# Kernel optimization log

Hardware: AMD Instinct MI355X
Metric: run time of the kernel (lower is better)

## Reference

```python
import math
import jax, jax.numpy as jnp
import numpy as np

V_NODES = 100000
N_EDGES = 1600000
EMBED = 768
HID = 256
H = 4
FH = HID // H
L = 2
PE_D = EMBED // 4  # 192
SLOPE = 0.2


def make_pe(max_len, d):
    pos = np.arange(max_len, dtype=np.float32)[:, None]
    div = np.exp(np.arange(0, d, 2, dtype=np.float32) * (-math.log(10000.0) / d))
    pe = np.zeros((max_len, d), dtype=np.float32)
    pe[:, 0::2] = np.sin(pos * div)
    pe[:, 1::2] = np.cos(pos * div)
    return jnp.asarray(pe)


def setup_inputs() -> dict:
    key = jax.random.key(0)
    ks = jax.random.split(key, 24)

    def xavier(k, shape):
        fan_in, fan_out = shape[0], shape[1]
        lim = math.sqrt(6.0 / (fan_in + fan_out))
        return jax.random.uniform(k, shape, jnp.float32, -lim, lim)

    in_proj_dim = EMBED + 2 * PE_D  # 1152
    inp = {
        'row_idx': jax.random.randint(ks[0], (V_NODES,), 0, 256),
        'col_idx': jax.random.randint(ks[1], (V_NODES,), 0, 64),
        'edge_index': jax.random.randint(ks[2], (2, N_EDGES), 0, V_NODES),
        'edge_weight': jax.random.uniform(ks[3], (N_EDGES,), jnp.float32),
        'W_in': xavier(ks[4], (in_proj_dim, HID)),
        'b_in': jnp.zeros((HID,), jnp.float32),
        'ln_g': jnp.ones((HID,), jnp.float32),
        'ln_b': jnp.zeros((HID,), jnp.float32),
        'Wq': jnp.stack([xavier(ks[5 + i], (HID, HID)) for i in range(L)]),
        'bq': jnp.zeros((L, HID), jnp.float32),
        'Wk': jnp.stack([xavier(ks[7 + i], (HID, HID)) for i in range(L)]),
        'bk': jnp.zeros((L, HID), jnp.float32),
        'Wv': jnp.stack([xavier(ks[9 + i], (HID, HID)) for i in range(L)]),
        'bv': jnp.zeros((L, HID), jnp.float32),
        'Wo': jnp.stack([xavier(ks[11 + i], (HID, HID)) for i in range(L)]),
        'bo': jnp.zeros((L, HID), jnp.float32),
        'We': jnp.stack([xavier(ks[13 + i], (1, H)) for i in range(L)]),  # edge_proj weight [1,H]
        'be': jnp.zeros((L, H), jnp.float32),
    }
    return inp


def gat_layer(h, src, tgt, ew, Wq, bq, Wk, bk, Wv, bv, Wo, bo, We, be):
    V = h.shape[0]
    Q = (h @ Wq + bq).reshape(V, H, FH)
    K = (h @ Wk + bk).reshape(V, H, FH)
    Vo = (h @ Wv + bv).reshape(V, H, FH)
    # edge bias: Linear(1,H) on edge_weight, then leaky relu -> [E,H]
    edge_bias = jax.nn.leaky_relu(ew[:, None] * We.reshape(1, H) + be, SLOPE)
    attn_raw = jnp.sum(Q[src] * K[tgt], axis=-1) / math.sqrt(FH) + edge_bias  # [E,H]
    attn_exp = jnp.exp(attn_raw)
    deg = jax.ops.segment_sum(attn_exp, tgt, num_segments=V) + 1e-16  # [V,H]
    attn_norm = attn_exp / deg[tgt]  # [E,H] (dropout is identity at eval)
    msg = Vo[src] * attn_norm[:, :, None] * ew[:, None, None]  # [E,H,FH]
    out = jax.ops.segment_sum(msg, tgt, num_segments=V).reshape(V, H * FH)
    return jax.nn.leaky_relu(out @ Wo + bo, SLOPE)


def reference(row_idx, col_idx, edge_index, edge_weight,
              W_in, b_in, ln_g, ln_b,
              Wq, bq, Wk, bk, Wv, bv, Wo, bo, We, be):
    V = row_idx.shape[0]
    row_pe = make_pe(256, PE_D)
    col_pe = make_pe(64, PE_D)
    cell = jnp.zeros((V, EMBED), jnp.float32)  # cell_embeds are zeros in source
    h = jnp.concatenate([cell, row_pe[row_idx], col_pe[col_idx]], axis=-1)
    # input_proj: Linear -> LayerNorm -> ReLU (dropout identity)
    h = h @ W_in + b_in
    mu = jnp.mean(h, axis=-1, keepdims=True)
    var = jnp.var(h, axis=-1, keepdims=True)
    h = (h - mu) / jnp.sqrt(var + 1e-5) * ln_g + ln_b
    h = jax.nn.relu(h)
    src, tgt = edge_index[0], edge_index[1]
    for i in range(L):
        h = gat_layer(h, src, tgt, edge_weight,
                      Wq[i], bq[i], Wk[i], bk[i], Wv[i], bv[i],
                      Wo[i], bo[i], We[i], be[i])
    return h
```

## Files before the change

### kernel.cpp

```cpp
#include <hip/hip_runtime.h>
#include <hip/hip_bf16.h>
#include <type_traits>
#include <math.h>

typedef __attribute__((ext_vector_type(8))) short bf16x8;
typedef __attribute__((ext_vector_type(4))) float f32x4;

__device__ __forceinline__ float bf2f(unsigned int u16) {
    union { unsigned int i; float f; } x; x.i = (u16 & 0xffffu) << 16; return x.f;
}
__device__ __forceinline__ unsigned int f2bf(float f) {
    union { float f; unsigned int i; } x; x.f = f;
    unsigned int i = x.i;
    unsigned int r = i + 0x7fffu + ((i >> 16) & 1u);
    return r >> 16;
}

#define SLOPE 0.2f

__global__ void k_hist(const int* __restrict__ tgt, int* __restrict__ cnt, int E) {
    int i = blockIdx.x * blockDim.x + threadIdx.x;
    if (i < E) atomicAdd(&cnt[tgt[i]], 1);
}

__global__ void __launch_bounds__(1024) k_scan1(const int* __restrict__ in, int* __restrict__ out,
                                                int* __restrict__ bsums, int n) {
    __shared__ int sm[1024];
    int i = blockIdx.x * 1024 + threadIdx.x;
    int v = (i < n) ? in[i] : 0;
    sm[threadIdx.x] = v; __syncthreads();
    for (int ofs = 1; ofs < 1024; ofs <<= 1) {
        int t = (threadIdx.x >= ofs) ? sm[threadIdx.x - ofs] : 0;
        __syncthreads();
        sm[threadIdx.x] += t;
        __syncthreads();
    }
    if (i < n) out[i] = sm[threadIdx.x];
    if (threadIdx.x == 1023) bsums[blockIdx.x] = sm[1023];
}

__global__ void __launch_bounds__(1024) k_scan2(int* bsums, int nb) {
    __shared__ int sm[1024];
    int v = (threadIdx.x < nb) ? bsums[threadIdx.x] : 0;
    sm[threadIdx.x] = v; __syncthreads();
    for (int ofs = 1; ofs < 1024; ofs <<= 1) {
        int t = (threadIdx.x >= ofs) ? sm[threadIdx.x - ofs] : 0;
        __syncthreads();
        sm[threadIdx.x] += t;
        __syncthreads();
    }
    if (threadIdx.x < nb) bsums[threadIdx.x] = sm[threadIdx.x] - v;
}

__global__ void __launch_bounds__(1024) k_scan3(int* __restrict__ out1, const int* __restrict__ bsums,
                                                int* __restrict__ off0, int n) {
    int i = blockIdx.x * 1024 + threadIdx.x;
    if (i < n) out1[i] += bsums[blockIdx.x];
    if (i == 0) off0[0] = 0;
}

__global__ void k_scatter(const int* __restrict__ ei, const float* __restrict__ ew,
                          const int* __restrict__ off, int* __restrict__ fill,
                          int* __restrict__ ssrc, float* __restrict__ sew, int E) {
    int e = blockIdx.x * blockDim.x + threadIdx.x;
    if (e < E) {
        int s = ei[e], t = ei[E + e];
        int pos = off[t] + atomicAdd(&fill[t], 1);
        ssrc[pos] = s; sew[pos] = ew[e];
    }
}

__global__ void k_combo(const int* __restrict__ ri, const int* __restrict__ ci,
                        int* __restrict__ combo, int V) {
    int v = blockIdx.x * blockDim.x + threadIdx.x;
    if (v < V) combo[v] = ri[v] * 64 + ci[v];
}

__global__ void __launch_bounds__(256) k_wt(const float* __restrict__ Wq, const float* __restrict__ Wk,
                                            const float* __restrict__ Wv, const float* __restrict__ Wo,
                                            unsigned short* __restrict__ WT) {
    __shared__ float sm[64][65];
    int blk = blockIdx.x;
    int m = blk >> 4, t = blk & 15;
    int tr = t >> 2, tc = t & 3;
    const float* srcs[4] = {Wq, Wk, Wv, Wo};
    const float* W = srcs[m & 3] + (size_t)(m >> 2) * 65536;
    int tid = threadIdx.x;
    for (int i = tid; i < 4096; i += 256) {
        int r = i >> 6, c = i & 63;
        sm[r][c] = W[(size_t)(tr * 64 + r) * 256 + tc * 64 + c];
    }
    __syncthreads();
    for (int i = tid; i < 4096; i += 256) {
        int n = i >> 6, k = i & 63;
        WT[(size_t)(m * 256 + tc * 64 + n) * 256 + tr * 64 + k] = (unsigned short)f2bf(sm[k][n]);
    }
}

__global__ void __launch_bounds__(256) k_bias(const float* __restrict__ bq, const float* __restrict__ bk,
                                              const float* __restrict__ bv, const float* __restrict__ bo,
                                              float* __restrict__ biasF) {
    int m = blockIdx.x, n = threadIdx.x;
    const float* srcs[4] = {bq, bk, bv, bo};
    biasF[m * 256 + n] = srcs[m & 3][(m >> 2) * 256 + n];
}

__global__ void __launch_bounds__(256) k_peproj(const float* __restrict__ W_in, float* __restrict__ AB) {
    __shared__ float pe[192];
    int blk = blockIdx.x;
    bool isA = blk < 256;
    int pos = isA ? blk : blk - 256;
    const float* Wb = W_in + (size_t)(isA ? 768 : 960) * 256;
    int tid = threadIdx.x;
    if (tid < 192) {
        float div = expf(-(float)(tid & ~1) * (logf(10000.0f) / 192.0f));
        float ang = (float)pos * div;
        pe[tid] = (tid & 1) ? cosf(ang) : sinf(ang);
    }
    __syncthreads();
    float acc = 0.f;
    #pragma unroll 8
    for (int d = 0; d < 192; ++d) acc = fmaf(pe[d], Wb[d * 256 + tid], acc);
    AB[blk * 256 + tid] = acc;
}

__global__ void __launch_bounds__(256) k_h0(const float* __restrict__ AB, const float* __restrict__ b_in,
                                            const float* __restrict__ g, const float* __restrict__ b,
                                            unsigned short* __restrict__ h0t) {
    int wid = threadIdx.x >> 6, lane = threadIdx.x & 63;
    int m = blockIdx.x * 4 + wid;
    int r = m >> 6, c = m & 63;
    float4 a  = ((const float4*)(AB + (size_t)r * 256))[lane];
    float4 bb = ((const float4*)(AB + (size_t)(256 + c) * 256))[lane];
    float4 bi = ((const float4*)b_in)[lane];
    float x0 = a.x + bb.x + bi.x, x1 = a.y + bb.y + bi.y;
    float x2 = a.z + bb.z + bi.z, x3 = a.w + bb.w + bi.w;
    float s = x0 + x1 + x2 + x3;
    #pragma unroll
    for (int msk = 1; msk < 64; msk <<= 1) s += __shfl_xor(s, msk);
    float mu = s * (1.f / 256.f);
    float d0 = x0 - mu, d1 = x1 - mu, d2 = x2 - mu, d3 = x3 - mu;
    float sq = d0 * d0 + d1 * d1 + d2 * d2 + d3 * d3;
    #pragma unroll
    for (int msk = 1; msk < 64; msk <<= 1) sq += __shfl_xor(sq, msk);
    float rstd = rsqrtf(sq * (1.f / 256.f) + 1e-5f);
    float4 gv = ((const float4*)g)[lane], bv = ((const float4*)b)[lane];
    float y0 = fmaxf(fmaf(d0 * rstd, gv.x, bv.x), 0.f);
    float y1 = fmaxf(fmaf(d1 * rstd, gv.y, bv.y), 0.f);
    float y2 = fmaxf(fmaf(d2 * rstd, gv.z, bv.z), 0.f);
    float y3 = fmaxf(fmaf(d3 * rstd, gv.w, bv.w), 0.f);
    uint2 o;
    o.x = f2bf(y0) | (f2bf(y1) << 16);
    o.y = f2bf(y2) | (f2bf(y3) << 16);
    *(uint2*)(h0t + (size_t)m * 256 + lane * 4) = o;
}

template <typename TC, bool LEAKY>
__global__ void __launch_bounds__(256) k_mm(const unsigned short* __restrict__ A,
                                            const unsigned short* __restrict__ WT,
                                            const float* __restrict__ bias,
                                            TC* __restrict__ C, int M, int ldc) {
    __shared__ __align__(16) unsigned short As[128][72];
    __shared__ __align__(16) unsigned short Bs[128][72];
    int tid = threadIdx.x;
    int R0 = blockIdx.x * 128, C0 = blockIdx.y * 128;
    int lane = tid & 63, wave = tid >> 6;
    int wr = (wave >> 1) * 64, wc = (wave & 1) * 64;
    int fr = lane & 15, fq = lane >> 4;
    f32x4 acc[4][4] = {};
    for (int k0 = 0; k0 < 256; k0 += 64) {
        for (int i = tid; i < 1024; i += 256) {
            int r = i >> 3, c8 = (i & 7) * 8;
            int gr = R0 + r;
            uint4 u = make_uint4(0u, 0u, 0u, 0u);
            if (gr < M) u = *(const uint4*)(A + (size_t)gr * 256 + k0 + c8);
            *(uint4*)&As[r][c8] = u;
            *(uint4*)&Bs[r][c8] = *(const uint4*)(WT + (size_t)(C0 + r) * 256 + k0 + c8);
        }
        __syncthreads();
        #pragma unroll
        for (int ks = 0; ks < 64; ks += 32) {
            bf16x8 af[4], bfv[4];
            #pragma unroll
            for (int mi = 0; mi < 4; ++mi) af[mi] = *(const bf16x8*)&As[wr + mi * 16 + fr][ks + fq * 8];
            #pragma unroll
            for (int ni = 0; ni < 4; ++ni) bfv[ni] = *(const bf16x8*)&Bs[wc + ni * 16 + fr][ks + fq * 8];
            #pragma unroll
            for (int mi = 0; mi < 4; ++mi)
                #pragma unroll
                for (int ni = 0; ni < 4; ++ni)
                    acc[mi][ni] = __builtin_amdgcn_mfma_f32_16x16x32_bf16(af[mi], bfv[ni], acc[mi][ni], 0, 0, 0);
        }
        __syncthreads();
    }
    #pragma unroll
    for (int mi = 0; mi < 4; ++mi) {
        #pragma unroll
        for (int r = 0; r < 4; ++r) {
            int row = R0 + wr + mi * 16 + fq * 4 + r;
            if (row >= M) continue;
            #pragma unroll
            for (int ni = 0; ni < 4; ++ni) {
                int col = C0 + wc + ni * 16 + fr;
                float v = acc[mi][ni][r] + bias[col];
                if (LEAKY) v = fmaxf(v, SLOPE * v);
                if constexpr (std::is_same<TC, float>::value) {
                    C[(size_t)row * ldc + col] = v;
                } else {
                    C[(size_t)row * ldc + col] = (unsigned short)f2bf(v);
                }
            }
        }
    }
}

template <bool USE_COMBO>
__global__ void __launch_bounds__(256) k_edge(const int* __restrict__ off, const int* __restrict__ ssrc,
                                              const float* __restrict__ sew, const int* __restrict__ combo,
                                              const unsigned short* __restrict__ QKV,
                                              const float* __restrict__ We_l, const float* __restrict__ be_l,
                                              unsigned short* __restrict__ out, int V) {
    int wid = threadIdx.x >> 6, lane = threadIdx.x & 63;
    int t = blockIdx.x * 4 + wid;
    if (t >= V) return;
    int q = lane & 15, quarter = lane >> 4;
    int h = q >> 2;
    int krow = USE_COMBO ? combo[t] : t;
    uint4 ka = *(const uint4*)(QKV + (size_t)krow * 768 + 256 + q * 16);
    uint4 kb = *(const uint4*)(QKV + (size_t)krow * 768 + 256 + q * 16 + 8);
    float kf[16];
    kf[0] = bf2f(ka.x); kf[1] = bf2f(ka.x >> 16); kf[2] = bf2f(ka.y); kf[3] = bf2f(ka.y >> 16);
    kf[4] = bf2f(ka.z); kf[5] = bf2f(ka.z >> 16); kf[6] = bf2f(ka.w); kf[7] = bf2f(ka.w >> 16);
    kf[8] = bf2f(kb.x); kf[9] = bf2f(kb.x >> 16); kf[10] = bf2f(kb.y); kf[11] = bf2f(kb.y >> 16);
    kf[12] = bf2f(kb.z); kf[13] = bf2f(kb.z >> 16); kf[14] = bf2f(kb.w); kf[15] = bf2f(kb.w >> 16);
    float Weh = We_l[h], beh = be_l[h];
    float n[16];
    #pragma unroll
    for (int j = 0; j < 16; ++j) n[j] = 0.f;
    float den = 0.f;
    int beg = off[t], end = off[t + 1];
    for (int e0 = beg; e0 < end; e0 += 64) {
        int nrem = end - e0; if (nrem > 64) nrem = 64;
        int sv = 0; float wv = 0.f;
        if (lane < nrem) {
            sv = ssrc[e0 + lane];
            wv = sew[e0 + lane];
            if (USE_COMBO) sv = combo[sv];
        }
        for (int i = 0; i < nrem; i += 4) {
            int ei = i + quarter;
            bool act = ei < nrem;
            int eidx = act ? ei : (nrem - 1);
            int srow = __shfl(sv, eidx);
            float w  = __shfl(wv, eidx);
            const unsigned short* base = QKV + (size_t)srow * 768 + q * 16;
            uint4 qa = *(const uint4*)base;
            uint4 qb = *(const uint4*)(base + 8);
            uint4 va = *(const uint4*)(base + 512);
            uint4 vb = *(const uint4*)(base + 520);
            float p;
            p = bf2f(qa.x) * kf[0];
            p = fmaf(bf2f(qa.x >> 16), kf[1], p);
            p = fmaf(bf2f(qa.y),       kf[2], p);
            p = fmaf(bf2f(qa.y >> 16), kf[3], p);
            p = fmaf(bf2f(qa.z),       kf[4], p);
            p = fmaf(bf2f(qa.z >> 16), kf[5], p);
            p = fmaf(bf2f(qa.w),       kf[6], p);
            p = fmaf(bf2f(qa.w >> 16), kf[7], p);
            p = fmaf(bf2f(qb.x),       kf[8], p);
            p = fmaf(bf2f(qb.x >> 16), kf[9], p);
            p = fmaf(bf2f(qb.y),       kf[10], p);
            p = fmaf(bf2f(qb.y >> 16), kf[11], p);
            p = fmaf(bf2f(qb.z),       kf[12], p);
            p = fmaf(bf2f(qb.z >> 16), kf[13], p);
            p = fmaf(bf2f(qb.w),       kf[14], p);
            p = fmaf(bf2f(qb.w >> 16), kf[15], p);
            p += __shfl_xor(p, 1);
            p += __shfl_xor(p, 2);
            float bias = fmaf(w, Weh, beh);
            bias = fmaxf(bias, SLOPE * bias);
            float ex = act ? __expf(fmaf(p, 0.125f, bias)) : 0.f;
            den += ex;
            float cc = ex * w;
            n[0]  = fmaf(cc, bf2f(va.x),       n[0]);
            n[1]  = fmaf(cc, bf2f(va.x >> 16), n[1]);
            n[2]  = fmaf(cc, bf2f(va.y),       n[2]);
            n[3]  = fmaf(cc, bf2f(va.y >> 16), n[3]);
            n[4]  = fmaf(cc, bf2f(va.z),       n[4]);
            n[5]  = fmaf(cc, bf2f(va.z >> 16), n[5]);
            n[6]  = fmaf(cc, bf2f(va.w),       n[6]);
            n[7]  = fmaf(cc, bf2f(va.w >> 16), n[7]);
            n[8]  = fmaf(cc, bf2f(vb.x),       n[8]);
            n[9]  = fmaf(cc, bf2f(vb.x >> 16), n[9]);
            n[10] = fmaf(cc, bf2f(vb.y),       n[10]);
            n[11] = fmaf(cc, bf2f(vb.y >> 16), n[11]);
            n[12] = fmaf(cc, bf2f(vb.z),       n[12]);
            n[13] = fmaf(cc, bf2f(vb.z >> 16), n[13]);
            n[14] = fmaf(cc, bf2f(vb.w),       n[14]);
            n[15] = fmaf(cc, bf2f(vb.w >> 16), n[15]);
        }
    }
    den += __shfl_xor(den, 16);
    den += __shfl_xor(den, 32);
    #pragma unroll
    for (int j = 0; j < 16; ++j) {
        n[j] += __shfl_xor(n[j], 16);
        n[j] += __shfl_xor(n[j], 32);
    }
    float inv = 1.f / (den + 1e-16f);
    if (quarter == 0) {
        uint4 o0, o1;
        o0.x = f2bf(n[0] * inv)  | (f2bf(n[1] * inv) << 16);
        o0.y = f2bf(n[2] * inv)  | (f2bf(n[3] * inv) << 16);
        o0.z = f2bf(n[4] * inv)  | (f2bf(n[5] * inv) << 16);
        o0.w = f2bf(n[6] * inv)  | (f2bf(n[7] * inv) << 16);
        o1.x = f2bf(n[8] * inv)  | (f2bf(n[9] * inv) << 16);
        o1.y = f2bf(n[10] * inv) | (f2bf(n[11] * inv) << 16);
        o1.z = f2bf(n[12] * inv) | (f2bf(n[13] * inv) << 16);
        o1.w = f2bf(n[14] * inv) | (f2bf(n[15] * inv) << 16);
        *(uint4*)(out + (size_t)t * 256 + q * 16) = o0;
        *(uint4*)(out + (size_t)t * 256 + q * 16 + 8) = o1;
    }
}

extern "C" void kernel_launch(void* const* d_in, const int* in_sizes, int n_in,
                              void* d_out, int out_size, void* d_ws, size_t ws_size,
                              hipStream_t stream) {
    const int*   row_idx = (const int*)d_in[0];
    const int*   col_idx = (const int*)d_in[1];
    const int*   ei      = (const int*)d_in[2];
    const float* ew      = (const float*)d_in[3];
    const float* W_in    = (const float*)d_in[4];
    const float* b_in    = (const float*)d_in[5];
    const float* ln_g    = (const float*)d_in[6];
    const float* ln_b    = (const float*)d_in[7];
    const float* Wq      = (const float*)d_in[8];
    const float* bq      = (const float*)d_in[9];
    const float* Wk      = (const float*)d_in[10];
    const float* bk      = (const float*)d_in[11];
    const float* Wv      = (const float*)d_in[12];
    const float* bv      = (const float*)d_in[13];
    const float* Wo      = (const float*)d_in[14];
    const float* bo      = (const float*)d_in[15];
    const float* We      = (const float*)d_in[16];
    const float* be      = (const float*)d_in[17];

    const int V = in_sizes[0];
    const int E = in_sizes[3];
    const int NC = 16384;

    char* w = (char*)d_ws;
    size_t o = 0;
    auto alloc = [&](size_t bytes) -> char* {
        char* p = w + o;
        o = (o + bytes + 255) & ~(size_t)255;
        return p;
    };
    int*   cnt     = (int*)alloc((size_t)V * 4);
    int*   fill    = (int*)alloc((size_t)V * 4);
    int*   csr_off = (int*)alloc((size_t)(V + 1) * 4);
    int*   bsums   = (int*)alloc(1024 * 4);
    int*   csr_src = (int*)alloc((size_t)E * 4);
    float* csr_ew  = (float*)alloc((size_t)E * 4);
    int*   combo   = (int*)alloc((size_t)V * 4);
    float* AB      = (float*)alloc((size_t)320 * 256 * 4);
    unsigned short* WT    = (unsigned short*)alloc((size_t)2048 * 256 * 2);
    float*          biasF = (float*)alloc((size_t)2048 * 4);
    unsigned short* h0t   = (unsigned short*)alloc((size_t)NC * 256 * 2);
    unsigned short* QKV1  = (unsigned short*)alloc((size_t)NC * 768 * 2);
    unsigned short* out_e = (unsigned short*)alloc((size_t)V * 256 * 2);
    unsigned short* h1    = (unsigned short*)alloc((size_t)V * 256 * 2);
    unsigned short* QKV2  = (unsigned short*)alloc((size_t)V * 768 * 2);

    hipMemsetAsync(cnt, 0, (size_t)V * 4, stream);
    hipMemsetAsync(fill, 0, (size_t)V * 4, stream);

    int eb = (E + 255) / 256;
    int nscan = (V + 1023) / 1024;
    k_hist<<<eb, 256, 0, stream>>>(ei + E, cnt, E);
    k_scan1<<<nscan, 1024, 0, stream>>>(cnt, csr_off + 1, bsums, V);
    k_scan2<<<1, 1024, 0, stream>>>(bsums, nscan);
    k_scan3<<<nscan, 1024, 0, stream>>>(csr_off + 1, bsums, csr_off, V);
    k_scatter<<<eb, 256, 0, stream>>>(ei, ew, csr_off, fill, csr_src, csr_ew, E);
    k_combo<<<(V + 255) / 256, 256, 0, stream>>>(row_idx, col_idx, combo, V);

    k_wt<<<128, 256, 0, stream>>>(Wq, Wk, Wv, Wo, WT);
    k_bias<<<8, 256, 0, stream>>>(bq, bk, bv, bo, biasF);
    k_peproj<<<320, 256, 0, stream>>>(W_in, AB);
    k_h0<<<NC / 4, 256, 0, stream>>>(AB, b_in, ln_g, ln_b, h0t);

    dim3 g1(NC / 128, 6);
    k_mm<unsigned short, false><<<g1, 256, 0, stream>>>(h0t, WT, biasF, QKV1, NC, 768);

    int tb = (V + 3) / 4;
    k_edge<true><<<tb, 256, 0, stream>>>(csr_off, csr_src, csr_ew, combo, QKV1, We, be, out_e, V);

    int mb = (V + 127) / 128;
    dim3 go(mb, 2);
    dim3 gqkv(mb, 6);
    k_mm<unsigned short, true><<<go, 256, 0, stream>>>(out_e, WT + (size_t)768 * 256, biasF + 768, h1, V, 256);
    k_mm<unsigned short, false><<<gqkv, 256, 0, stream>>>(h1, WT + (size_t)1024 * 256, biasF + 1024, QKV2, V, 768);

    k_edge<false><<<tb, 256, 0, stream>>>(csr_off, csr_src, csr_ew, combo, QKV2, We + 4, be + 4, out_e, V);

    k_mm<float, true><<<go, 256, 0, stream>>>(out_e, WT + (size_t)1792 * 256, biasF + 1792, (float*)d_out, V, 256);
}
```

Measured before the change: 861.1 us.

## Pack CSR edges as int2 with pre-resolved combo and widen GEMM N tile

```diff
diff --git a/kernel.cpp b/kernel.cpp
--- a/kernel.cpp
+++ b/kernel.cpp
@@ -59,21 +59,24 @@
     if (i == 0) off0[0] = 0;
 }
 
+__global__ void k_combo(const int* __restrict__ ri, const int* __restrict__ ci,
+                        int* __restrict__ combo, int V) {
+    int v = blockIdx.x * blockDim.x + threadIdx.x;
+    if (v < V) combo[v] = ri[v] * 64 + ci[v];
+}
+
 __global__ void k_scatter(const int* __restrict__ ei, const float* __restrict__ ew,
                           const int* __restrict__ off, int* __restrict__ fill,
-                          int* __restrict__ ssrc, float* __restrict__ sew, int E) {
+                          const int* __restrict__ combo,
+                          int2* __restrict__ p1, int2* __restrict__ p2, int E) {
     int e = blockIdx.x * blockDim.x + threadIdx.x;
     if (e < E) {
         int s = ei[e], t = ei[E + e];
         int pos = off[t] + atomicAdd(&fill[t], 1);
-        ssrc[pos] = s; sew[pos] = ew[e];
-    }
-}
-
-__global__ void k_combo(const int* __restrict__ ri, const int* __restrict__ ci,
-                        int* __restrict__ combo, int V) {
-    int v = blockIdx.x * blockDim.x + threadIdx.x;
-    if (v < V) combo[v] = ri[v] * 64 + ci[v];
+        int wbits = __float_as_int(ew[e]);
+        p1[pos] = make_int2(combo[s], wbits);
+        p2[pos] = make_int2(s, wbits);
+    }
 }
 
 __global__ void __launch_bounds__(256) k_wt(const float* __restrict__ Wq, const float* __restrict__ Wk,
@@ -161,13 +164,13 @@
                                             const float* __restrict__ bias,
                                             TC* __restrict__ C, int M, int ldc) {
     __shared__ __align__(16) unsigned short As[128][72];
-    __shared__ __align__(16) unsigned short Bs[128][72];
+    __shared__ __align__(16) unsigned short Bs[256][72];
     int tid = threadIdx.x;
-    int R0 = blockIdx.x * 128, C0 = blockIdx.y * 128;
+    int R0 = blockIdx.x * 128, C0 = blockIdx.y * 256;
     int lane = tid & 63, wave = tid >> 6;
-    int wr = (wave >> 1) * 64, wc = (wave & 1) * 64;
+    int wr = (wave >> 1) * 64, wc = (wave & 1) * 128;
     int fr = lane & 15, fq = lane >> 4;
-    f32x4 acc[4][4] = {};
+    f32x4 acc[4][8] = {};
     for (int k0 = 0; k0 < 256; k0 += 64) {
         for (int i = tid; i < 1024; i += 256) {
             int r = i >> 3, c8 = (i & 7) * 8;
@@ -175,20 +178,23 @@
             uint4 u = make_uint4(0u, 0u, 0u, 0u);
             if (gr < M) u = *(const uint4*)(A + (size_t)gr * 256 + k0 + c8);
             *(uint4*)&As[r][c8] = u;
+        }
+        for (int i = tid; i < 2048; i += 256) {
+            int r = i >> 3, c8 = (i & 7) * 8;
             *(uint4*)&Bs[r][c8] = *(const uint4*)(WT + (size_t)(C0 + r) * 256 + k0 + c8);
         }
         __syncthreads();
         #pragma unroll
         for (int ks = 0; ks < 64; ks += 32) {
-            bf16x8 af[4], bfv[4];
+            bf16x8 af[4], bfv[8];
             #pragma unroll
             for (int mi = 0; mi < 4; ++mi) af[mi] = *(const bf16x8*)&As[wr + mi * 16 + fr][ks + fq * 8];
             #pragma unroll
-            for (int ni = 0; ni < 4; ++ni) bfv[ni] = *(const bf16x8*)&Bs[wc + ni * 16 + fr][ks + fq * 8];
+            for (int ni = 0; ni < 8; ++ni) bfv[ni] = *(const bf16x8*)&Bs[wc + ni * 16 + fr][ks + fq * 8];
             #pragma unroll
             for (int mi = 0; mi < 4; ++mi)
                 #pragma unroll
-                for (int ni = 0; ni < 4; ++ni)
+                for (int ni = 0; ni < 8; ++ni)
                     acc[mi][ni] = __builtin_amdgcn_mfma_f32_16x16x32_bf16(af[mi], bfv[ni], acc[mi][ni], 0, 0, 0);
         }
         __syncthreads();
@@ -200,7 +206,7 @@
             int row = R0 + wr + mi * 16 + fq * 4 + r;
             if (row >= M) continue;
             #pragma unroll
-            for (int ni = 0; ni < 4; ++ni) {
+            for (int ni = 0; ni < 8; ++ni) {
                 int col = C0 + wc + ni * 16 + fr;
                 float v = acc[mi][ni][r] + bias[col];
                 if (LEAKY) v = fmaxf(v, SLOPE * v);
@@ -215,8 +221,8 @@
 }
 
 template <bool USE_COMBO>
-__global__ void __launch_bounds__(256) k_edge(const int* __restrict__ off, const int* __restrict__ ssrc,
-                                              const float* __restrict__ sew, const int* __restrict__ combo,
+__global__ void __launch_bounds__(256) k_edge(const int* __restrict__ off, const int2* __restrict__ pedge,
+                                              const int* __restrict__ combo,
                                               const unsigned short* __restrict__ QKV,
                                               const float* __restrict__ We_l, const float* __restrict__ be_l,
                                               unsigned short* __restrict__ out, int V) {
@@ -243,9 +249,9 @@
         int nrem = end - e0; if (nrem > 64) nrem = 64;
         int sv = 0; float wv = 0.f;
         if (lane < nrem) {
-            sv = ssrc[e0 + lane];
-            wv = sew[e0 + lane];
-            if (USE_COMBO) sv = combo[sv];
+            int2 pr = pedge[e0 + lane];
+            sv = pr.x;
+            wv = __int_as_float(pr.y);
         }
         for (int i = 0; i < nrem; i += 4) {
             int ei = i + quarter;
@@ -360,8 +366,8 @@
     int*   fill    = (int*)alloc((size_t)V * 4);
     int*   csr_off = (int*)alloc((size_t)(V + 1) * 4);
     int*   bsums   = (int*)alloc(1024 * 4);
-    int*   csr_src = (int*)alloc((size_t)E * 4);
-    float* csr_ew  = (float*)alloc((size_t)E * 4);
+    int2*  csrP1   = (int2*)alloc((size_t)E * 8);
+    int2*  csrP2   = (int2*)alloc((size_t)E * 8);
     int*   combo   = (int*)alloc((size_t)V * 4);
     float* AB      = (float*)alloc((size_t)320 * 256 * 4);
     unsigned short* WT    = (unsigned short*)alloc((size_t)2048 * 256 * 2);
@@ -381,27 +387,27 @@
     k_scan1<<<nscan, 1024, 0, stream>>>(cnt, csr_off + 1, bsums, V);
     k_scan2<<<1, 1024, 0, stream>>>(bsums, nscan);
     k_scan3<<<nscan, 1024, 0, stream>>>(csr_off + 1, bsums, csr_off, V);
-    k_scatter<<<eb, 256, 0, stream>>>(ei, ew, csr_off, fill, csr_src, csr_ew, E);
     k_combo<<<(V + 255) / 256, 256, 0, stream>>>(row_idx, col_idx, combo, V);
+    k_scatter<<<eb, 256, 0, stream>>>(ei, ew, csr_off, fill, combo, csrP1, csrP2, E);
 
     k_wt<<<128, 256, 0, stream>>>(Wq, Wk, Wv, Wo, WT);
     k_bias<<<8, 256, 0, stream>>>(bq, bk, bv, bo, biasF);
     k_peproj<<<320, 256, 0, stream>>>(W_in, AB);
     k_h0<<<NC / 4, 256, 0, stream>>>(AB, b_in, ln_g, ln_b, h0t);
 
-    dim3 g1(NC / 128, 6);
+    dim3 g1(NC / 128, 3);
     k_mm<unsigned short, false><<<g1, 256, 0, stream>>>(h0t, WT, biasF, QKV1, NC, 768);
 
     int tb = (V + 3) / 4;
-    k_edge<true><<<tb, 256, 0, stream>>>(csr_off, csr_src, csr_ew, combo, QKV1, We, be, out_e, V);
+    k_edge<true><<<tb, 256, 0, stream>>>(csr_off, csrP1, combo, QKV1, We, be, out_e, V);
 
     int mb = (V + 127) / 128;
-    dim3 go(mb, 2);
-    dim3 gqkv(mb, 6);
+    dim3 go(mb, 1);
+    dim3 gqkv(mb, 3);
     k_mm<unsigned short, true><<<go, 256, 0, stream>>>(out_e, WT + (size_t)768 * 256, biasF + 768, h1, V, 256);
     k_mm<unsigned short, false><<<gqkv, 256, 0, stream>>>(h1, WT + (size_t)1024 * 256, biasF + 1024, QKV2, V, 768);
 
-    k_edge<false><<<tb, 256, 0, stream>>>(csr_off, csr_src, csr_ew, combo, QKV2, We + 4, be + 4, out_e, V);
+    k_edge<false><<<tb, 256, 0, stream>>>(csr_off, csrP2, combo, QKV2, We + 4, be + 4, out_e, V);
 
     k_mm<float, true><<<go, 256, 0, stream>>>(out_e, WT + (size_t)1792 * 256, biasF + 1792, (float*)d_out, V, 256);
 }
```

New measurement: 1.023 ms. 1.19x slower.

## Use direct global-to-LDS loads with XOR swizzle in GEMM, pack CSR edges

Applied to the files above, without the earlier changes.

```diff
diff --git a/kernel.cpp b/kernel.cpp
--- a/kernel.cpp
+++ b/kernel.cpp
@@ -5,6 +5,9 @@
 
 typedef __attribute__((ext_vector_type(8))) short bf16x8;
 typedef __attribute__((ext_vector_type(4))) float f32x4;
+
+typedef __attribute__((address_space(3))) char       lds_char;
+typedef const __attribute__((address_space(1))) char g_char;
 
 __device__ __forceinline__ float bf2f(unsigned int u16) {
     union { unsigned int i; float f; } x; x.i = (u16 & 0xffffu) << 16; return x.f;
@@ -59,21 +62,21 @@
     if (i == 0) off0[0] = 0;
 }
 
+__global__ void k_combo(const int* __restrict__ ri, const int* __restrict__ ci,
+                        int* __restrict__ combo, int V) {
+    int v = blockIdx.x * blockDim.x + threadIdx.x;
+    if (v < V) combo[v] = ri[v] * 64 + ci[v];
+}
+
 __global__ void k_scatter(const int* __restrict__ ei, const float* __restrict__ ew,
                           const int* __restrict__ off, int* __restrict__ fill,
-                          int* __restrict__ ssrc, float* __restrict__ sew, int E) {
+                          int2* __restrict__ p, int E) {
     int e = blockIdx.x * blockDim.x + threadIdx.x;
     if (e < E) {
         int s = ei[e], t = ei[E + e];
         int pos = off[t] + atomicAdd(&fill[t], 1);
-        ssrc[pos] = s; sew[pos] = ew[e];
-    }
-}
-
-__global__ void k_combo(const int* __restrict__ ri, const int* __restrict__ ci,
-                        int* __restrict__ combo, int V) {
-    int v = blockIdx.x * blockDim.x + threadIdx.x;
-    if (v < V) combo[v] = ri[v] * 64 + ci[v];
+        p[pos] = make_int2(s, __float_as_int(ew[e]));
+    }
 }
 
 __global__ void __launch_bounds__(256) k_wt(const float* __restrict__ Wq, const float* __restrict__ Wk,
@@ -160,8 +163,8 @@
                                             const unsigned short* __restrict__ WT,
                                             const float* __restrict__ bias,
                                             TC* __restrict__ C, int M, int ldc) {
-    __shared__ __align__(16) unsigned short As[128][72];
-    __shared__ __align__(16) unsigned short Bs[128][72];
+    __shared__ __align__(16) char AsB[16384];
+    __shared__ __align__(16) char BsB[16384];
     int tid = threadIdx.x;
     int R0 = blockIdx.x * 128, C0 = blockIdx.y * 128;
     int lane = tid & 63, wave = tid >> 6;
@@ -169,22 +172,36 @@
     int fr = lane & 15, fq = lane >> 4;
     f32x4 acc[4][4] = {};
     for (int k0 = 0; k0 < 256; k0 += 64) {
-        for (int i = tid; i < 1024; i += 256) {
-            int r = i >> 3, c8 = (i & 7) * 8;
+        #pragma unroll
+        for (int it = 0; it < 4; ++it) {
+            int chunk = it * 256 + tid;
+            int r = chunk >> 3, cb = (chunk & 7) * 16;
+            int sc = cb ^ ((r & 7) << 4);
             int gr = R0 + r;
-            uint4 u = make_uint4(0u, 0u, 0u, 0u);
-            if (gr < M) u = *(const uint4*)(A + (size_t)gr * 256 + k0 + c8);
-            *(uint4*)&As[r][c8] = u;
-            *(uint4*)&Bs[r][c8] = *(const uint4*)(WT + (size_t)(C0 + r) * 256 + k0 + c8);
+            if (gr < M)
+                __builtin_amdgcn_global_load_lds(
+                    (g_char*)((const char*)(A + (size_t)gr * 256 + k0) + sc),
+                    (lds_char*)(AsB + (size_t)(it * 256 + wave * 64) * 16), 16, 0, 0);
+            __builtin_amdgcn_global_load_lds(
+                (g_char*)((const char*)(WT + (size_t)(C0 + r) * 256 + k0) + sc),
+                (lds_char*)(BsB + (size_t)(it * 256 + wave * 64) * 16), 16, 0, 0);
         }
         __syncthreads();
         #pragma unroll
-        for (int ks = 0; ks < 64; ks += 32) {
+        for (int ks = 0; ks < 2; ++ks) {
             bf16x8 af[4], bfv[4];
             #pragma unroll
-            for (int mi = 0; mi < 4; ++mi) af[mi] = *(const bf16x8*)&As[wr + mi * 16 + fr][ks + fq * 8];
+            for (int mi = 0; mi < 4; ++mi) {
+                int r = wr + mi * 16 + fr;
+                int kb = ks * 64 + fq * 16;
+                af[mi] = *(const bf16x8*)(AsB + r * 128 + (kb ^ ((r & 7) << 4)));
+            }
             #pragma unroll
-            for (int ni = 0; ni < 4; ++ni) bfv[ni] = *(const bf16x8*)&Bs[wc + ni * 16 + fr][ks + fq * 8];
+            for (int ni = 0; ni < 4; ++ni) {
+                int r = wc + ni * 16 + fr;
+                int kb = ks * 64 + fq * 16;
+                bfv[ni] = *(const bf16x8*)(BsB + r * 128 + (kb ^ ((r & 7) << 4)));
+            }
             #pragma unroll
             for (int mi = 0; mi < 4; ++mi)
                 #pragma unroll
@@ -215,8 +232,8 @@
 }
 
 template <bool USE_COMBO>
-__global__ void __launch_bounds__(256) k_edge(const int* __restrict__ off, const int* __restrict__ ssrc,
-                                              const float* __restrict__ sew, const int* __restrict__ combo,
+__global__ void __launch_bounds__(256) k_edge(const int* __restrict__ off, const int2* __restrict__ pedge,
+                                              const int* __restrict__ combo,
                                               const unsigned short* __restrict__ QKV,
                                               const float* __restrict__ We_l, const float* __restrict__ be_l,
                                               unsigned short* __restrict__ out, int V) {
@@ -243,8 +260,9 @@
         int nrem = end - e0; if (nrem > 64) nrem = 64;
         int sv = 0; float wv = 0.f;
         if (lane < nrem) {
-            sv = ssrc[e0 + lane];
-            wv = sew[e0 + lane];
+            int2 pr = pedge[e0 + lane];
+            sv = pr.x;
+            wv = __int_as_float(pr.y);
             if (USE_COMBO) sv = combo[sv];
         }
         for (int i = 0; i < nrem; i += 4) {
@@ -360,8 +378,7 @@
     int*   fill    = (int*)alloc((size_t)V * 4);
     int*   csr_off = (int*)alloc((size_t)(V + 1) * 4);
     int*   bsums   = (int*)alloc(1024 * 4);
-    int*   csr_src = (int*)alloc((size_t)E * 4);
-    float* csr_ew  = (float*)alloc((size_t)E * 4);
+    int2*  csrP    = (int2*)alloc((size_t)E * 8);
     int*   combo   = (int*)alloc((size_t)V * 4);
     float* AB      = (float*)alloc((size_t)320 * 256 * 4);
     unsigned short* WT    = (unsigned short*)alloc((size_t)2048 * 256 * 2);
@@ -381,8 +398,8 @@
     k_scan1<<<nscan, 1024, 0, stream>>>(cnt, csr_off + 1, bsums, V);
     k_scan2<<<1, 1024, 0, stream>>>(bsums, nscan);
     k_scan3<<<nscan, 1024, 0, stream>>>(csr_off + 1, bsums, csr_off, V);
-    k_scatter<<<eb, 256, 0, stream>>>(ei, ew, csr_off, fill, csr_src, csr_ew, E);
     k_combo<<<(V + 255) / 256, 256, 0, stream>>>(row_idx, col_idx, combo, V);
+    k_scatter<<<eb, 256, 0, stream>>>(ei, ew, csr_off, fill, csrP, E);
 
     k_wt<<<128, 256, 0, stream>>>(Wq, Wk, Wv, Wo, WT);
     k_bias<<<8, 256, 0, stream>>>(bq, bk, bv, bo, biasF);
@@ -393,7 +410,7 @@
     k_mm<unsigned short, false><<<g1, 256, 0, stream>>>(h0t, WT, biasF, QKV1, NC, 768);
 
     int tb = (V + 3) / 4;
-    k_edge<true><<<tb, 256, 0, stream>>>(csr_off, csr_src, csr_ew, combo, QKV1, We, be, out_e, V);
+    k_edge<true><<<tb, 256, 0, stream>>>(csr_off, csrP, combo, QKV1, We, be, out_e, V);
 
     int mb = (V + 127) / 128;
     dim3 go(mb, 2);
@@ -401,7 +418,7 @@
     k_mm<unsigned short, true><<<go, 256, 0, stream>>>(out_e, WT + (size_t)768 * 256, biasF + 768, h1, V, 256);
     k_mm<unsigned short, false><<<gqkv, 256, 0, stream>>>(h1, WT + (size_t)1024 * 256, biasF + 1024, QKV2, V, 768);
 
-    k_edge<false><<<tb, 256, 0, stream>>>(csr_off, csr_src, csr_ew, combo, QKV2, We + 4, be + 4, out_e, V);
+    k_edge<false><<<tb, 256, 0, stream>>>(csr_off, csrP, combo, QKV2, We + 4, be + 4, out_e, V);
 
     k_mm<float, true><<<go, 256, 0, stream>>>(out_e, WT + (size_t)1792 * 256, biasF + 1792, (float*)d_out, V, 256);
 }
```

Result: faster. 788.6 us (-8.4%).
